# Optimization experiments

Measured on AMD Instinct MI355X. Metric: run time of the kernel, lower is better.

## Reference

```python
import jax, jax.numpy as jnp
import numpy as np

IN_F = 1024
OUT_F = 1024
N_ORDER = 13  # grid_size=10 + spline_order=3
RMS_EPS = 1e-6


def setup_inputs() -> dict:
    key = jax.random.key(0)
    k_x, k_b, k_p = jax.random.split(key, 3)
    x = jax.random.normal(k_x, (4, 2048, IN_F), dtype=jnp.float32)
    # flax param init: normal(stddev=scale_base/sqrt(in_features)) etc.
    base_weight = jax.random.normal(k_b, (IN_F, OUT_F), dtype=jnp.float32) * (1.0 / np.sqrt(IN_F))
    poly_weight = jax.random.normal(k_p, (N_ORDER, IN_F, OUT_F), dtype=jnp.float32) * (0.1 / np.sqrt(IN_F * N_ORDER))
    rms_scale = jnp.ones((OUT_F,), dtype=jnp.float32)  # nn.RMSNorm default scale init
    return {"x": x, "base_weight": base_weight, "poly_weight": poly_weight, "rms_scale": rms_scale}


def reference(x, base_weight, poly_weight, rms_scale):
    orig_dtype = x.dtype
    prefix = x.shape[:-1]
    x_2d = x.reshape(-1, IN_F)  # [B, in]

    # Base path: SiLU(x) @ W_base in bf16
    x_c = x_2d.astype(jnp.bfloat16)
    out = jax.nn.silu(x_c) @ base_weight.astype(jnp.bfloat16)  # [B, out] bf16

    # Chebyshev recursion on tanh-normalized fp32 input
    x_safe = jnp.tanh(x_2d.astype(jnp.float32))
    pw = poly_weight.astype(jnp.bfloat16)
    T_prev = jnp.ones_like(x_safe)
    T_curr = x_safe
    out = out + T_prev.astype(jnp.bfloat16) @ pw[0]
    out = out + T_curr.astype(jnp.bfloat16) @ pw[1]
    for k in range(2, N_ORDER):  # fixed small unroll (13 orders)
        T_next = 2.0 * x_safe * T_curr - T_prev
        out = out + T_next.astype(jnp.bfloat16) @ pw[k]
        T_prev = T_curr
        T_curr = T_next

    # RMSNorm (flax default: eps=1e-6, learned scale)
    o32 = out.astype(jnp.float32)
    ms = jnp.mean(o32 * o32, axis=-1, keepdims=True)
    o32 = o32 * jax.lax.rsqrt(ms + RMS_EPS) * rms_scale
    return o32.astype(orig_dtype).reshape(prefix + (OUT_F,))
```

## Files before the change

kernel.cpp:

```cpp
#include <hip/hip_runtime.h>
#include <cstdint>

#define IN_F  1024
#define OUT_F 1024
#define NORD  13
#define BROWS 8192

typedef __bf16 bf16x8 __attribute__((ext_vector_type(8)));
typedef float  f32x4  __attribute__((ext_vector_type(4)));
typedef unsigned short u16x8 __attribute__((ext_vector_type(8)));
typedef unsigned short u16x4 __attribute__((ext_vector_type(4)));

__device__ __forceinline__ unsigned short f2bf(float f) {
  unsigned int u = __float_as_uint(f);
  unsigned int r = u + 0x7FFFu + ((u >> 16) & 1u);
  return (unsigned short)(r >> 16);
}
__device__ __forceinline__ float bf2f(unsigned short h) {
  return __uint_as_float(((unsigned int)h) << 16);
}
__device__ __forceinline__ float bfround(float f) { return bf2f(f2bf(f)); }

__device__ __forceinline__ void gload_lds16(const void* g, void* l) {
  __builtin_amdgcn_global_load_lds(
      (__attribute__((address_space(1))) unsigned int*)(uintptr_t)g,
      (__attribute__((address_space(3))) unsigned int*)(unsigned int)(uintptr_t)l,
      16, 0, 0);
}

__global__ __launch_bounds__(256)
void prep_kernel(const float* __restrict__ x, const float* __restrict__ baseW,
                 const float* __restrict__ poly, unsigned short* __restrict__ A,
                 unsigned short* __restrict__ Wt, float* __restrict__ partial,
                 int b0, int nb, int Kp) {
  int bid = blockIdx.x;
  int t   = threadIdx.x;

  if (bid < 4096) {
    int row = bid * 2 + (t >> 7);
    int f0  = (t & 127) * 8;
    const float* xr = x + (size_t)row * IN_F + f0;
    float xv[8];
    *(float4*)&xv[0] = *(const float4*)&xr[0];
    *(float4*)&xv[4] = *(const float4*)&xr[4];
    unsigned short* Ar = A + (size_t)row * Kp;
    int omax = b0 + nb - 1;
    if (b0 == 0) {
      u16x8 sv;
#pragma unroll
      for (int i = 0; i < 8; i++) {
        float xc = bfround(xv[i]);
        float sg = bfround(1.0f / (1.0f + expf(-xc)));
        sv[i] = f2bf(xc * sg);
      }
      *(u16x8*)&Ar[f0] = sv;
    }
    float xs[8], tp[8], tc[8];
#pragma unroll
    for (int i = 0; i < 8; i++) { xs[i] = tanhf(xv[i]); tp[i] = 1.0f; tc[i] = xs[i]; }
    for (int o = 1; o <= omax; o++) {
      if (o >= b0) {
        int bb = o - b0;
        u16x8 sv;
#pragma unroll
        for (int i = 0; i < 8; i++) sv[i] = f2bf(tc[i]);
        *(u16x8*)&Ar[(size_t)bb * 1024 + f0] = sv;
      }
      {
#pragma clang fp contract(off)
#pragma unroll
        for (int i = 0; i < 8; i++) {
          float tm = 2.0f * xs[i] * tc[i];
          float tn = tm - tp[i];
          tp[i] = tc[i]; tc[i] = tn;
        }
      }
    }
    return;
  }

  if (bid < 4096 + 256 * nb) {
    __shared__ float tile[64][65];
    int w   = bid - 4096;
    int bb  = w >> 8;
    int rem = w & 255;
    int n0  = (rem & 15) * 64;
    int f0  = (rem >> 4) * 64;
    int g   = b0 + bb;
    const float* src = (g == 0) ? baseW : (poly + (size_t)g * (IN_F * OUT_F));
    int fl = t >> 4, n4 = (t & 15) * 4;
#pragma unroll
    for (int i = 0; i < 4; i++) {
      int f = fl + 16 * i;
      float4 v = *(const float4*)&src[(size_t)(f0 + f) * OUT_F + n0 + n4];
      tile[f][n4 + 0] = v.x; tile[f][n4 + 1] = v.y;
      tile[f][n4 + 2] = v.z; tile[f][n4 + 3] = v.w;
    }
    __syncthreads();
    int f8 = (t & 7) * 8, nl = t >> 3;
#pragma unroll
    for (int i = 0; i < 2; i++) {
      int n = nl + 32 * i;
      u16x8 o;
#pragma unroll
      for (int j = 0; j < 8; j++) o[j] = f2bf(tile[f8 + j][n]);
      *(u16x8*)&Wt[(size_t)(n0 + n) * Kp + (size_t)bb * 1024 + f0 + f8] = o;
    }
    return;
  }

  int w2 = bid - (4096 + 256 * nb);
  int n  = (w2 & 3) * 256 + t;
  int fc = w2 >> 2;
  float s = 0.f;
  for (int f = fc * 128; f < fc * 128 + 128; f++)
    s += bf2f(f2bf(poly[(size_t)f * OUT_F + n]));
  partial[(size_t)fc * OUT_F + n] = s;
}

__global__ __launch_bounds__(256, 2)
void gemm_kernel(const unsigned short* __restrict__ A, const unsigned short* __restrict__ Wt,
                 unsigned short* __restrict__ outAcc, const float* __restrict__ partial,
                 int Kp, int isFirst) {
  __shared__ unsigned short sA[2][128 * 64];
  __shared__ unsigned short sB[2][128 * 64];
  int t    = threadIdx.x;
  int m0   = blockIdx.x * 128;
  int n0   = blockIdx.y * 128;
  int wave = t >> 6, lane = t & 63;
  int lr   = lane & 15, quad = lane >> 4;
  int wm   = (wave & 1) * 64, wn = (wave >> 1) * 64;

  int rs = t >> 3;
  int jg = (t & 7) ^ (rs & 7);
  const unsigned short* aSrc = A  + (size_t)(m0 + rs) * Kp + jg * 8;
  const unsigned short* bSrc = Wt + (size_t)(n0 + rs) * Kp + jg * 8;
  char* sAc = (char*)sA;
  char* sBc = (char*)sB;
  int ldsOff = t * 16;

  int aOff[4][2], bOff[4][2];
#pragma unroll
  for (int mi = 0; mi < 4; mi++) {
    int row = wm + mi * 16 + lr;
#pragma unroll
    for (int ks = 0; ks < 2; ks++) {
      int j = ks * 4 + quad;
      aOff[mi][ks] = row * 128 + ((j ^ (row & 7)) * 16);
    }
  }
#pragma unroll
  for (int ni = 0; ni < 4; ni++) {
    int row = wn + ni * 16 + lr;
#pragma unroll
    for (int ks = 0; ks < 2; ks++) {
      int j = ks * 4 + quad;
      bOff[ni][ks] = row * 128 + ((j ^ (row & 7)) * 16);
    }
  }

  f32x4 s[4][4];
  float bsr[4];
  if (isFirst) {
#pragma unroll
    for (int ni = 0; ni < 4; ni++) {
      int gn = n0 + wn + ni * 16 + lr;
      float bsum = 0.f;
#pragma unroll
      for (int fc = 0; fc < 8; fc++) bsum += partial[(size_t)fc * OUT_F + gn];
      bsr[ni] = bfround(bsum);
    }
  } else {
#pragma unroll
    for (int ni = 0; ni < 4; ni++) {
      int gn = n0 + wn + ni * 16 + lr;
#pragma unroll
      for (int mi = 0; mi < 4; mi++) {
        int gmBase = m0 + wm + mi * 16 + quad * 4;
#pragma unroll
        for (int r = 0; r < 4; r++)
          s[mi][ni][r] = bf2f(outAcc[(size_t)(gmBase + r) * OUT_F + gn]);
      }
    }
  }

  int nKt  = Kp >> 6;
  int nBlk = Kp >> 10;

  auto stage = [&](int gkt, int buf) {
    const unsigned short* aP = aSrc + gkt * 64;
    const unsigned short* bP = bSrc + gkt * 64;
    char* dA = sAc + buf * 16384 + ldsOff;
    char* dB = sBc + buf * 16384 + ldsOff;
#pragma unroll
    for (int rd = 0; rd < 4; rd++)
      gload_lds16(aP + (size_t)rd * 32 * Kp, dA + rd * 4096);
#pragma unroll
    for (int rd = 0; rd < 4; rd++)
      gload_lds16(bP + (size_t)rd * 32 * Kp, dB + rd * 4096);
  };

  stage(0, 0);

  int gkt = 0;
  for (int blk = 0; blk < nBlk; blk++) {
    f32x4 acc[4][4];
#pragma unroll
    for (int mi = 0; mi < 4; mi++)
#pragma unroll
      for (int ni = 0; ni < 4; ni++)
        acc[mi][ni] = (f32x4){0.f, 0.f, 0.f, 0.f};

    for (int kt = 0; kt < 16; kt++, gkt++) {
      __syncthreads();
      int nxt = gkt + 1;
      if (nxt < nKt) stage(nxt, nxt & 1);
      int buf = gkt & 1;
      char* bA = sAc + buf * 16384;
      char* bB = sBc + buf * 16384;
#pragma unroll
      for (int ks = 0; ks < 2; ks++) {
        bf16x8 af[4], bfr[4];
#pragma unroll
        for (int mi = 0; mi < 4; mi++) af[mi] = *(const bf16x8*)(bA + aOff[mi][ks]);
#pragma unroll
        for (int ni = 0; ni < 4; ni++) bfr[ni] = *(const bf16x8*)(bB + bOff[ni][ks]);
#pragma unroll
        for (int mi = 0; mi < 4; mi++)
#pragma unroll
          for (int ni = 0; ni < 4; ni++)
            acc[mi][ni] = __builtin_amdgcn_mfma_f32_16x16x32_bf16(af[mi], bfr[ni], acc[mi][ni], 0, 0, 0);
      }
    }

    bool firstBlk = (isFirst && blk == 0);
    if (firstBlk) {
#pragma unroll
      for (int mi = 0; mi < 4; mi++)
#pragma unroll
        for (int ni = 0; ni < 4; ni++)
#pragma unroll
          for (int r = 0; r < 4; r++) {
            float p = bfround(acc[mi][ni][r]);
            s[mi][ni][r] = bfround(p + bsr[ni]);
          }
    } else {
#pragma unroll
      for (int mi = 0; mi < 4; mi++)
#pragma unroll
        for (int ni = 0; ni < 4; ni++)
#pragma unroll
          for (int r = 0; r < 4; r++)
            s[mi][ni][r] = bfround(s[mi][ni][r] + bfround(acc[mi][ni][r]));
    }
  }

#pragma unroll
  for (int ni = 0; ni < 4; ni++) {
    int gn = n0 + wn + ni * 16 + lr;
#pragma unroll
    for (int mi = 0; mi < 4; mi++) {
      int gmBase = m0 + wm + mi * 16 + quad * 4;
#pragma unroll
      for (int r = 0; r < 4; r++)
        outAcc[(size_t)(gmBase + r) * OUT_F + gn] = f2bf(s[mi][ni][r]);
    }
  }
}

__global__ __launch_bounds__(256)
void rms_kernel(const unsigned short* __restrict__ outAcc, const float* __restrict__ scale,
                float* __restrict__ out) {
  int row = blockIdx.x;
  int t   = threadIdx.x;
  const unsigned short* src = outAcc + (size_t)row * OUT_F;
  u16x4 hv = *(const u16x4*)&src[t * 4];
  float v[4];
#pragma unroll
  for (int i = 0; i < 4; i++) v[i] = bf2f(hv[i]);
  float s = v[0]*v[0] + v[1]*v[1] + v[2]*v[2] + v[3]*v[3];
#pragma unroll
  for (int off = 32; off > 0; off >>= 1) s += __shfl_down(s, off, 64);
  __shared__ float red[4];
  if ((t & 63) == 0) red[t >> 6] = s;
  __syncthreads();
  float tot = red[0] + red[1] + red[2] + red[3];
  float sc = 1.0f / sqrtf(tot * (1.0f / OUT_F) + 1e-6f);
  float4 so = *(const float4*)&scale[t * 4];
  float4 o;
  o.x = v[0] * sc * so.x; o.y = v[1] * sc * so.y;
  o.z = v[2] * sc * so.z; o.w = v[3] * sc * so.w;
  *(float4*)&out[(size_t)row * OUT_F + t * 4] = o;
}

extern "C" void kernel_launch(void* const* d_in, const int* in_sizes, int n_in,
                              void* d_out, int out_size, void* d_ws, size_t ws_size,
                              hipStream_t stream) {
  const float* x     = (const float*)d_in[0];
  const float* baseW = (const float*)d_in[1];
  const float* poly  = (const float*)d_in[2];
  const float* scale = (const float*)d_in[3];
  float* out = (float*)d_out;

  char* ws = (char*)d_ws;
  unsigned short* outAcc = (unsigned short*)ws;
  float* partial = (float*)(ws + 16777216);
  size_t fixed   = 16777216 + 32768;

  int CHB = 1;
  for (int c = NORD; c >= 1; c--) {
    size_t need = fixed + (size_t)c * 1024 * OUT_F * 2
                + (size_t)BROWS * c * 1024 * 2;
    if (need <= ws_size) { CHB = c; break; }
  }
  unsigned short* Wt = (unsigned short*)(ws + fixed);
  unsigned short* Ap = (unsigned short*)(ws + fixed + (size_t)CHB * 1024 * OUT_F * 2);

  for (int b0 = 0; b0 < NORD; b0 += CHB) {
    int nb = (CHB < NORD - b0) ? CHB : (NORD - b0);
    int Kp = nb * 1024;
    int nBias = (b0 == 0) ? 32 : 0;
    prep_kernel<<<4096 + 256 * nb + nBias, 256, 0, stream>>>(x, baseW, poly, Ap, Wt, partial, b0, nb, Kp);
    gemm_kernel<<<dim3(BROWS / 128, 8), 256, 0, stream>>>(Ap, Wt, outAcc, partial, Kp, (b0 == 0) ? 1 : 0);
  }
  rms_kernel<<<BROWS, 256, 0, stream>>>(outAcc, scale, out);
}
```

Before: 437.8 us.

## Split prep kernel, halve GEMM K-tile, pack running sums to raise occupancy

Splits the fused prep kernel into separate activation, weight-transpose and bias kernels, the last launched once up front. The GEMM K tile drops from 64 to 32, halving LDS per block, and occupancy is raised to 3 blocks per CU. Running sums are now held as packed bf16 pairs rather than fp32, cutting register pressure. The aim is better latency hiding at higher occupancy, at the cost of twice as many barrier-synchronised k-steps with less MFMA work between them.

```diff
diff --git a/kernel.cpp b/kernel.cpp
--- a/kernel.cpp
+++ b/kernel.cpp
@@ -29,101 +29,96 @@
 }
 
 __global__ __launch_bounds__(256)
-void prep_kernel(const float* __restrict__ x, const float* __restrict__ baseW,
-                 const float* __restrict__ poly, unsigned short* __restrict__ A,
-                 unsigned short* __restrict__ Wt, float* __restrict__ partial,
-                 int b0, int nb, int Kp) {
-  int bid = blockIdx.x;
+void act_kernel(const float* __restrict__ x, unsigned short* __restrict__ A,
+                int b0, int nb, int Kp) {
   int t   = threadIdx.x;
-
-  if (bid < 4096) {
-    int row = bid * 2 + (t >> 7);
-    int f0  = (t & 127) * 8;
-    const float* xr = x + (size_t)row * IN_F + f0;
-    float xv[8];
-    *(float4*)&xv[0] = *(const float4*)&xr[0];
-    *(float4*)&xv[4] = *(const float4*)&xr[4];
-    unsigned short* Ar = A + (size_t)row * Kp;
-    int omax = b0 + nb - 1;
-    if (b0 == 0) {
+  int row = blockIdx.x * 2 + (t >> 7);
+  int f0  = (t & 127) * 8;
+  const float* xr = x + (size_t)row * IN_F + f0;
+  float xv[8];
+  *(float4*)&xv[0] = *(const float4*)&xr[0];
+  *(float4*)&xv[4] = *(const float4*)&xr[4];
+  unsigned short* Ar = A + (size_t)row * Kp;
+  int omax = b0 + nb - 1;
+  if (b0 == 0) {
+    u16x8 sv;
+#pragma unroll
+    for (int i = 0; i < 8; i++) {
+      float xc = bfround(xv[i]);
+      float sg = bfround(1.0f / (1.0f + expf(-xc)));
+      sv[i] = f2bf(xc * sg);
+    }
+    *(u16x8*)&Ar[f0] = sv;
+  }
+  float xs[8], tp[8], tc[8];
+#pragma unroll
+  for (int i = 0; i < 8; i++) { xs[i] = tanhf(xv[i]); tp[i] = 1.0f; tc[i] = xs[i]; }
+  for (int o = 1; o <= omax; o++) {
+    if (o >= b0) {
+      int bb = o - b0;
       u16x8 sv;
 #pragma unroll
+      for (int i = 0; i < 8; i++) sv[i] = f2bf(tc[i]);
+      *(u16x8*)&Ar[(size_t)bb * 1024 + f0] = sv;
+    }
+    {
+#pragma clang fp contract(off)
+#pragma unroll
       for (int i = 0; i < 8; i++) {
-        float xc = bfround(xv[i]);
-        float sg = bfround(1.0f / (1.0f + expf(-xc)));
-        sv[i] = f2bf(xc * sg);
+        float tm = 2.0f * xs[i] * tc[i];
+        float tn = tm - tp[i];
+        tp[i] = tc[i]; tc[i] = tn;
       }
-      *(u16x8*)&Ar[f0] = sv;
-    }
-    float xs[8], tp[8], tc[8];
-#pragma unroll
-    for (int i = 0; i < 8; i++) { xs[i] = tanhf(xv[i]); tp[i] = 1.0f; tc[i] = xs[i]; }
-    for (int o = 1; o <= omax; o++) {
-      if (o >= b0) {
-        int bb = o - b0;
-        u16x8 sv;
-#pragma unroll
-        for (int i = 0; i < 8; i++) sv[i] = f2bf(tc[i]);
-        *(u16x8*)&Ar[(size_t)bb * 1024 + f0] = sv;
-      }
-      {
-#pragma clang fp contract(off)
-#pragma unroll
-        for (int i = 0; i < 8; i++) {
-          float tm = 2.0f * xs[i] * tc[i];
-          float tn = tm - tp[i];
-          tp[i] = tc[i]; tc[i] = tn;
-        }
-      }
-    }
-    return;
-  }
-
-  if (bid < 4096 + 256 * nb) {
-    __shared__ float tile[64][65];
-    int w   = bid - 4096;
-    int bb  = w >> 8;
-    int rem = w & 255;
-    int n0  = (rem & 15) * 64;
-    int f0  = (rem >> 4) * 64;
-    int g   = b0 + bb;
-    const float* src = (g == 0) ? baseW : (poly + (size_t)g * (IN_F * OUT_F));
-    int fl = t >> 4, n4 = (t & 15) * 4;
-#pragma unroll
-    for (int i = 0; i < 4; i++) {
-      int f = fl + 16 * i;
-      float4 v = *(const float4*)&src[(size_t)(f0 + f) * OUT_F + n0 + n4];
-      tile[f][n4 + 0] = v.x; tile[f][n4 + 1] = v.y;
-      tile[f][n4 + 2] = v.z; tile[f][n4 + 3] = v.w;
-    }
-    __syncthreads();
-    int f8 = (t & 7) * 8, nl = t >> 3;
-#pragma unroll
-    for (int i = 0; i < 2; i++) {
-      int n = nl + 32 * i;
-      u16x8 o;
-#pragma unroll
-      for (int j = 0; j < 8; j++) o[j] = f2bf(tile[f8 + j][n]);
-      *(u16x8*)&Wt[(size_t)(n0 + n) * Kp + (size_t)bb * 1024 + f0 + f8] = o;
-    }
-    return;
-  }
-
-  int w2 = bid - (4096 + 256 * nb);
-  int n  = (w2 & 3) * 256 + t;
-  int fc = w2 >> 2;
+    }
+  }
+}
+
+__global__ __launch_bounds__(256)
+void wprep_kernel(const float* __restrict__ baseW, const float* __restrict__ poly,
+                  unsigned short* __restrict__ Wt, int b0, int Kp) {
+  __shared__ float tile[64][65];
+  int bb = blockIdx.z;
+  int g  = b0 + bb;
+  const float* src = (g == 0) ? baseW : (poly + (size_t)g * (IN_F * OUT_F));
+  int n0 = blockIdx.x * 64, f0 = blockIdx.y * 64;
+  int t  = threadIdx.x;
+  int fl = t >> 4, n4 = (t & 15) * 4;
+#pragma unroll
+  for (int i = 0; i < 4; i++) {
+    int f = fl + 16 * i;
+    float4 v = *(const float4*)&src[(size_t)(f0 + f) * OUT_F + n0 + n4];
+    tile[f][n4 + 0] = v.x; tile[f][n4 + 1] = v.y;
+    tile[f][n4 + 2] = v.z; tile[f][n4 + 3] = v.w;
+  }
+  __syncthreads();
+  int f8 = (t & 7) * 8, nl = t >> 3;
+#pragma unroll
+  for (int i = 0; i < 2; i++) {
+    int n = nl + 32 * i;
+    u16x8 o;
+#pragma unroll
+    for (int j = 0; j < 8; j++) o[j] = f2bf(tile[f8 + j][n]);
+    *(u16x8*)&Wt[(size_t)(n0 + n) * Kp + (size_t)bb * 1024 + f0 + f8] = o;
+  }
+}
+
+__global__ __launch_bounds__(256)
+void bias1_kernel(const float* __restrict__ pw0, float* __restrict__ partial) {
+  int t  = threadIdx.x;
+  int n  = blockIdx.x * 256 + t;
+  int fc = blockIdx.y;
   float s = 0.f;
   for (int f = fc * 128; f < fc * 128 + 128; f++)
-    s += bf2f(f2bf(poly[(size_t)f * OUT_F + n]));
+    s += bf2f(f2bf(pw0[(size_t)f * OUT_F + n]));
   partial[(size_t)fc * OUT_F + n] = s;
 }
 
-__global__ __launch_bounds__(256, 2)
+__global__ __launch_bounds__(256, 3)
 void gemm_kernel(const unsigned short* __restrict__ A, const unsigned short* __restrict__ Wt,
                  unsigned short* __restrict__ outAcc, const float* __restrict__ partial,
                  int Kp, int isFirst) {
-  __shared__ unsigned short sA[2][128 * 64];
-  __shared__ unsigned short sB[2][128 * 64];
+  __shared__ unsigned short sA[2][128 * 32];
+  __shared__ unsigned short sB[2][128 * 32];
   int t    = threadIdx.x;
   int m0   = blockIdx.x * 128;
   int n0   = blockIdx.y * 128;
@@ -131,35 +126,27 @@
   int lr   = lane & 15, quad = lane >> 4;
   int wm   = (wave & 1) * 64, wn = (wave >> 1) * 64;
 
-  int rs = t >> 3;
-  int jg = (t & 7) ^ (rs & 7);
+  int rs = t >> 2;
+  int jg = (t & 3) ^ (rs & 3);
   const unsigned short* aSrc = A  + (size_t)(m0 + rs) * Kp + jg * 8;
   const unsigned short* bSrc = Wt + (size_t)(n0 + rs) * Kp + jg * 8;
   char* sAc = (char*)sA;
   char* sBc = (char*)sB;
   int ldsOff = t * 16;
 
-  int aOff[4][2], bOff[4][2];
+  int aOff[4], bOff[4];
 #pragma unroll
   for (int mi = 0; mi < 4; mi++) {
     int row = wm + mi * 16 + lr;
-#pragma unroll
-    for (int ks = 0; ks < 2; ks++) {
-      int j = ks * 4 + quad;
-      aOff[mi][ks] = row * 128 + ((j ^ (row & 7)) * 16);
-    }
+    aOff[mi] = row * 64 + ((quad ^ (row & 3)) * 16);
   }
 #pragma unroll
   for (int ni = 0; ni < 4; ni++) {
     int row = wn + ni * 16 + lr;
-#pragma unroll
-    for (int ks = 0; ks < 2; ks++) {
-      int j = ks * 4 + quad;
-      bOff[ni][ks] = row * 128 + ((j ^ (row & 7)) * 16);
-    }
-  }
-
-  f32x4 s[4][4];
+    bOff[ni] = row * 64 + ((quad ^ (row & 3)) * 16);
+  }
+
+  unsigned int sp[4][4][2];
   float bsr[4];
   if (isFirst) {
 #pragma unroll
@@ -178,31 +165,34 @@
       for (int mi = 0; mi < 4; mi++) {
         int gmBase = m0 + wm + mi * 16 + quad * 4;
 #pragma unroll
-        for (int r = 0; r < 4; r++)
-          s[mi][ni][r] = bf2f(outAcc[(size_t)(gmBase + r) * OUT_F + gn]);
+        for (int p = 0; p < 2; p++) {
+          unsigned int lo = outAcc[(size_t)(gmBase + 2 * p) * OUT_F + gn];
+          unsigned int hi = outAcc[(size_t)(gmBase + 2 * p + 1) * OUT_F + gn];
+          sp[mi][ni][p] = lo | (hi << 16);
+        }
       }
     }
   }
 
-  int nKt  = Kp >> 6;
+  int nKt = Kp >> 5;
+
+  auto stage = [&](int gkt, int buf) {
+    const unsigned short* aP = aSrc + gkt * 32;
+    const unsigned short* bP = bSrc + gkt * 32;
+    char* dA = sAc + buf * 8192 + ldsOff;
+    char* dB = sBc + buf * 8192 + ldsOff;
+#pragma unroll
+    for (int rd = 0; rd < 2; rd++)
+      gload_lds16(aP + (size_t)rd * 64 * Kp, dA + rd * 4096);
+#pragma unroll
+    for (int rd = 0; rd < 2; rd++)
+      gload_lds16(bP + (size_t)rd * 64 * Kp, dB + rd * 4096);
+  };
+
+  stage(0, 0);
+
+  int gkt = 0;
   int nBlk = Kp >> 10;
-
-  auto stage = [&](int gkt, int buf) {
-    const unsigned short* aP = aSrc + gkt * 64;
-    const unsigned short* bP = bSrc + gkt * 64;
-    char* dA = sAc + buf * 16384 + ldsOff;
-    char* dB = sBc + buf * 16384 + ldsOff;
-#pragma unroll
-    for (int rd = 0; rd < 4; rd++)
-      gload_lds16(aP + (size_t)rd * 32 * Kp, dA + rd * 4096);
-#pragma unroll
-    for (int rd = 0; rd < 4; rd++)
-      gload_lds16(bP + (size_t)rd * 32 * Kp, dB + rd * 4096);
-  };
-
-  stage(0, 0);
-
-  int gkt = 0;
   for (int blk = 0; blk < nBlk; blk++) {
     f32x4 acc[4][4];
 #pragma unroll
@@ -211,48 +201,45 @@
       for (int ni = 0; ni < 4; ni++)
         acc[mi][ni] = (f32x4){0.f, 0.f, 0.f, 0.f};
 
-    for (int kt = 0; kt < 16; kt++, gkt++) {
+    for (int kt = 0; kt < 32; kt++, gkt++) {
       __syncthreads();
       int nxt = gkt + 1;
       if (nxt < nKt) stage(nxt, nxt & 1);
       int buf = gkt & 1;
-      char* bA = sAc + buf * 16384;
-      char* bB = sBc + buf * 16384;
-#pragma unroll
-      for (int ks = 0; ks < 2; ks++) {
-        bf16x8 af[4], bfr[4];
-#pragma unroll
-        for (int mi = 0; mi < 4; mi++) af[mi] = *(const bf16x8*)(bA + aOff[mi][ks]);
-#pragma unroll
-        for (int ni = 0; ni < 4; ni++) bfr[ni] = *(const bf16x8*)(bB + bOff[ni][ks]);
-#pragma unroll
-        for (int mi = 0; mi < 4; mi++)
-#pragma unroll
-          for (int ni = 0; ni < 4; ni++)
-            acc[mi][ni] = __builtin_amdgcn_mfma_f32_16x16x32_bf16(af[mi], bfr[ni], acc[mi][ni], 0, 0, 0);
-      }
+      char* bA = sAc + buf * 8192;
+      char* bB = sBc + buf * 8192;
+      bf16x8 af[4], bfr[4];
+#pragma unroll
+      for (int mi = 0; mi < 4; mi++) af[mi] = *(const bf16x8*)(bA + aOff[mi]);
+#pragma unroll
+      for (int ni = 0; ni < 4; ni++) bfr[ni] = *(const bf16x8*)(bB + bOff[ni]);
+#pragma unroll
+      for (int mi = 0; mi < 4; mi++)
+#pragma unroll
+        for (int ni = 0; ni < 4; ni++)
+          acc[mi][ni] = __builtin_amdgcn_mfma_f32_16x16x32_bf16(af[mi], bfr[ni], acc[mi][ni], 0, 0, 0);
     }
 
     bool firstBlk = (isFirst && blk == 0);
-    if (firstBlk) {
-#pragma unroll
-      for (int mi = 0; mi < 4; mi++)
-#pragma unroll
-        for (int ni = 0; ni < 4; ni++)
-#pragma unroll
-          for (int r = 0; r < 4; r++) {
-            float p = bfround(acc[mi][ni][r]);
-            s[mi][ni][r] = bfround(p + bsr[ni]);
+#pragma unroll
+    for (int mi = 0; mi < 4; mi++)
+#pragma unroll
+      for (int ni = 0; ni < 4; ni++)
+#pragma unroll
+        for (int p = 0; p < 2; p++) {
+          float a0 = bfround(acc[mi][ni][2 * p]);
+          float a1 = bfround(acc[mi][ni][2 * p + 1]);
+          float s0, s1;
+          if (firstBlk) {
+            s0 = bfround(a0 + bsr[ni]);
+            s1 = bfround(a1 + bsr[ni]);
+          } else {
+            unsigned int w = sp[mi][ni][p];
+            s0 = bfround(bf2f((unsigned short)(w & 0xffff)) + a0);
+            s1 = bfround(bf2f((unsigned short)(w >> 16)) + a1);
           }
-    } else {
-#pragma unroll
-      for (int mi = 0; mi < 4; mi++)
-#pragma unroll
-        for (int ni = 0; ni < 4; ni++)
-#pragma unroll
-          for (int r = 0; r < 4; r++)
-            s[mi][ni][r] = bfround(s[mi][ni][r] + bfround(acc[mi][ni][r]));
-    }
+          sp[mi][ni][p] = (unsigned int)f2bf(s0) | ((unsigned int)f2bf(s1) << 16);
+        }
   }
 
 #pragma unroll
@@ -262,8 +249,11 @@
     for (int mi = 0; mi < 4; mi++) {
       int gmBase = m0 + wm + mi * 16 + quad * 4;
 #pragma unroll
-      for (int r = 0; r < 4; r++)
-        outAcc[(size_t)(gmBase + r) * OUT_F + gn] = f2bf(s[mi][ni][r]);
+      for (int p = 0; p < 2; p++) {
+        unsigned int w = sp[mi][ni][p];
+        outAcc[(size_t)(gmBase + 2 * p) * OUT_F + gn]     = (unsigned short)(w & 0xffff);
+        outAcc[(size_t)(gmBase + 2 * p + 1) * OUT_F + gn] = (unsigned short)(w >> 16);
+      }
     }
   }
 }
@@ -316,11 +306,13 @@
   unsigned short* Wt = (unsigned short*)(ws + fixed);
   unsigned short* Ap = (unsigned short*)(ws + fixed + (size_t)CHB * 1024 * OUT_F * 2);
 
+  bias1_kernel<<<dim3(4, 8), 256, 0, stream>>>(poly, partial);
+
   for (int b0 = 0; b0 < NORD; b0 += CHB) {
     int nb = (CHB < NORD - b0) ? CHB : (NORD - b0);
     int Kp = nb * 1024;
-    int nBias = (b0 == 0) ? 32 : 0;
-    prep_kernel<<<4096 + 256 * nb + nBias, 256, 0, stream>>>(x, baseW, poly, Ap, Wt, partial, b0, nb, Kp);
+    act_kernel<<<BROWS / 2, 256, 0, stream>>>(x, Ap, b0, nb, Kp);
+    wprep_kernel<<<dim3(16, 16, nb), 256, 0, stream>>>(baseW, poly, Wt, b0, Kp);
     gemm_kernel<<<dim3(BROWS / 128, 8), 256, 0, stream>>>(Ap, Wt, outAcc, partial, Kp, (b0 == 0) ? 1 : 0);
   }
   rms_kernel<<<BROWS, 256, 0, stream>>>(outAcc, scale, out);
```

New measurement: 465.2 us. 6.3% more time.
